# Kernel optimization log

Hardware: AMD Instinct MI355X
Metric: run time of the kernel (lower is better)

Reference implementation:

```python
import jax, jax.numpy as jnp
import numpy as np

N_WORD, N_DOC, E = 20000, 20000, 500000
H, O, D = 4, 32, 128  # heads, out per head, hidden*heads
NEG_SLOPE = 0.2


def setup_inputs() -> dict:
    key = jax.random.key(0)
    ks = jax.random.split(key, 24)
    rn = lambda k, s, sc=0.1: jax.random.normal(k, s, dtype=jnp.float32) * sc
    ri = lambda k, s, hi: jax.random.randint(k, s, 0, hi, dtype=jnp.int32)
    return {
        'x_word': rn(ks[0], (N_WORD, 300), 1.0),
        'x_doc': rn(ks[1], (N_DOC, D), 1.0),
        'Wp_word': rn(ks[2], (300, D)), 'bp_word': jnp.zeros((D,), jnp.float32),
        'Wp_doc': rn(ks[3], (D, D)), 'bp_doc': jnp.zeros((D,), jnp.float32),
        'Wsrc': rn(ks[4], (2, 3, D, D)), 'bsrc': jnp.zeros((2, 3, D), jnp.float32),
        'Wdst': rn(ks[5], (2, 3, D, D)), 'bdst': jnp.zeros((2, 3, D), jnp.float32),
        'attn': rn(ks[6], (2, 3, H, O)), 'bconv': jnp.zeros((2, 3, D), jnp.float32),
        'Wc1': rn(ks[7], (D, 64)), 'bc1': jnp.zeros((64,), jnp.float32),
        'Wc2': rn(ks[8], (64, 64)), 'bc2': jnp.zeros((64,), jnp.float32),
        'src_wd': ri(ks[9], (E,), N_WORD), 'dst_wd': ri(ks[10], (E,), N_DOC),
        'src_dw': ri(ks[11], (E,), N_DOC), 'dst_dw': ri(ks[12], (E,), N_WORD),
        'src_dd': ri(ks[13], (E,), N_DOC), 'dst_dd': ri(ks[14], (E,), N_DOC),
    }


def _gatv2(h_src, h_dst, src, dst, Ws, bs, Wd, bd, a, bias, n_dst):
    # GATv2Conv (DGL): e = a . leaky_relu(Ws h_u + Wd h_v); edge softmax per dst; sum alpha*Ws h_u
    fs = (h_src @ Ws + bs).reshape(-1, H, O)           # [N_src,H,O]
    fd = (h_dst @ Wd + bd).reshape(-1, H, O)           # [N_dst,H,O]
    e = jax.nn.leaky_relu(fs[src] + fd[dst], NEG_SLOPE)  # [E,H,O]
    score = jnp.einsum('eho,ho->eh', e, a)             # [E,H]
    m = jax.lax.stop_gradient(jax.ops.segment_max(score, dst, num_segments=n_dst))
    ex = jnp.exp(score - m[dst])
    s = jax.ops.segment_sum(ex, dst, num_segments=n_dst)
    alpha = ex / s[dst]                                 # per-dst softmax
    rst = jax.ops.segment_sum(alpha[:, :, None] * fs[src], dst, num_segments=n_dst)
    return rst + bias.reshape(1, H, O)


def reference(x_word, x_doc, Wp_word, bp_word, Wp_doc, bp_doc, Wsrc, bsrc, Wdst, bdst,
              attn, bconv, Wc1, bc1, Wc2, bc2, src_wd, dst_wd, src_dw, dst_dw, src_dd, dst_dd):
    h_w = x_word @ Wp_word + bp_word
    h_d = x_doc @ Wp_doc + bp_doc
    for l in range(2):
        o_wd = _gatv2(h_w, h_d, src_wd, dst_wd, Wsrc[l, 0], bsrc[l, 0], Wdst[l, 0], bdst[l, 0], attn[l, 0], bconv[l, 0], N_DOC)
        o_dw = _gatv2(h_d, h_w, src_dw, dst_dw, Wsrc[l, 1], bsrc[l, 1], Wdst[l, 1], bdst[l, 1], attn[l, 1], bconv[l, 1], N_WORD)
        o_dd = _gatv2(h_d, h_d, src_dd, dst_dd, Wsrc[l, 2], bsrc[l, 2], Wdst[l, 2], bdst[l, 2], attn[l, 2], bconv[l, 2], N_DOC)
        h_d = ((o_wd + o_dd) * 0.5).reshape(N_DOC, D)   # mean over 2 relations into 'document'
        h_w = o_dw.reshape(N_WORD, D)                    # mean over 1 relation into 'word'
    z = jax.nn.relu(h_d @ Wc1 + bc1)
    return z @ Wc2 + bc2  # [N_DOC, len_label]
```

## Files before the change

kernel.cpp:

```cpp
#include <hip/hip_runtime.h>

#define NNODE 20000
#define NEDGE 500000
#define CAP 64

typedef __attribute__((ext_vector_type(8))) short bf16x8;
typedef __attribute__((ext_vector_type(8))) unsigned short u16x8;
typedef __attribute__((ext_vector_type(4))) float f32x4;
typedef __attribute__((ext_vector_type(4))) int i32x4;

__device__ __forceinline__ unsigned short f2bf(float f) {
    unsigned u = __float_as_uint(f);
    return (unsigned short)((u + 0x7FFFu + ((u >> 16) & 1u)) >> 16);
}
__device__ __forceinline__ float bf2f(unsigned short h) {
    return __uint_as_float((unsigned)h << 16);
}

__device__ __forceinline__ void split_row4(
    const float* __restrict__ X, unsigned short* __restrict__ A2,
    int K, int Kp, int r, int c)
{
    float v[4];
#pragma unroll
    for (int j = 0; j < 4; ++j) v[j] = (c + j < K) ? X[(size_t)r * K + c + j] : 0.f;
    ushort4 hi, lo;
    unsigned short h;
    h = f2bf(v[0]); hi.x = h; lo.x = f2bf(v[0] - bf2f(h));
    h = f2bf(v[1]); hi.y = h; lo.y = f2bf(v[1] - bf2f(h));
    h = f2bf(v[2]); hi.z = h; lo.z = f2bf(v[2] - bf2f(h));
    h = f2bf(v[3]); hi.w = h; lo.w = f2bf(v[3] - bf2f(h));
    *reinterpret_cast<ushort4*>(A2 + (size_t)r * 2 * Kp + c) = hi;
    *reinterpret_cast<ushort4*>(A2 + (size_t)r * 2 * Kp + Kp + c) = lo;
}

__global__ __launch_bounds__(256) void split_x_kernel(
    const float* __restrict__ xw, const float* __restrict__ xd,
    unsigned short* __restrict__ Ax, unsigned short* __restrict__ Axd)
{
    int i = blockIdx.x * 256 + threadIdx.x;
    const int T1 = NNODE * 80;
    const int T2 = NNODE * 32;
    if (i < T1) {
        int r = i / 80, c = (i % 80) * 4;
        split_row4(xw, Ax, 300, 320, r, c);
    } else if (i < T1 + T2) {
        i -= T1;
        int r = i / 32, c = (i % 32) * 4;
        split_row4(xd, Axd, 128, 128, r, c);
    }
}

__device__ __forceinline__ void split_one(
    const float* __restrict__ B, unsigned short* __restrict__ Bt,
    int K, int N, int Kp, int i)
{
    int n = i / Kp, k = i % Kp;
    float v = (k < K) ? B[(size_t)k * N + n] : 0.f;
    unsigned short h = f2bf(v);
    Bt[i] = h;
    Bt[(size_t)N * Kp + i] = f2bf(v - bf2f(h));
}

__global__ __launch_bounds__(256) void prep_weights_kernel(
    const float* __restrict__ Wp_word, const float* __restrict__ Wp_doc,
    const float* __restrict__ Wsrc, const float* __restrict__ Wdst,
    const float* __restrict__ Wc1, const float* __restrict__ Wc2,
    unsigned short* __restrict__ WtPw, unsigned short* __restrict__ WtPd,
    unsigned short* __restrict__ WtCat,
    unsigned short* __restrict__ WtC1, unsigned short* __restrict__ WtC2)
{
    int i = blockIdx.x * 256 + threadIdx.x;
    const int S0 = 128 * 320, S1 = 128 * 128, S2 = 6 * 256 * 128;
    const int S3 = 64 * 128, S4 = 64 * 64;
    if (i < S0) { split_one(Wp_word, WtPw, 300, 128, 320, i); return; }
    i -= S0;
    if (i < S1) { split_one(Wp_doc, WtPd, 128, 128, 128, i); return; }
    i -= S1;
    if (i < S2) {
        int lc = i / (256 * 128), rem = i % (256 * 128);
        int n = rem / 128, k = rem % 128;
        int l = lc / 3, c = lc % 3;
        int half = n >> 7, nn = n & 127;
        const float* M;
        if (c == 0)      M = half ? (Wdst + (size_t)(l * 3 + 1) * 16384) : (Wsrc + (size_t)(l * 3 + 0) * 16384);
        else if (c == 1) M = half ? (Wsrc + (size_t)(l * 3 + 1) * 16384) : (Wdst + (size_t)(l * 3 + 0) * 16384);
        else             M = half ? (Wdst + (size_t)(l * 3 + 2) * 16384) : (Wsrc + (size_t)(l * 3 + 2) * 16384);
        float v = M[(size_t)k * 128 + nn];
        unsigned short h = f2bf(v);
        unsigned short* Bt = WtCat + (size_t)lc * 65536;
        Bt[(size_t)n * 128 + k] = h;
        Bt[32768 + (size_t)n * 128 + k] = f2bf(v - bf2f(h));
        return;
    }
    i -= S2;
    if (i < S3) { split_one(Wc1, WtC1, 128, 64, 128, i); return; }
    i -= S3;
    if (i < S4) { split_one(Wc2, WtC2, 64, 64, 64, i); }
}

template<int BM, int BN, int MODE>
__global__ __launch_bounds__(512) void gemm_mfma_kernel(
    const unsigned short* __restrict__ A2,
    const unsigned short* __restrict__ Bt,
    const float* __restrict__ b0,
    float* __restrict__ C0, unsigned short* __restrict__ S0,
    int M, int Kp, int do_relu)
{
    constexpr int FM = BM / 32;
    constexpr int FN = BN / 64;
    __shared__ unsigned short As[2][BM][40];
    __shared__ unsigned short Bs[2][BN][40];
    const int tid = threadIdx.x;
    const int m0 = blockIdx.x * BM;
    const int wid = tid >> 6, lane = tid & 63;
    const int wm = wid >> 2, wn = wid & 3;
    const int lr = lane & 15, kg = lane >> 4;

    f32x4 acc[FM][FN] = {};
    const size_t KA = 2 * (size_t)Kp;
    const size_t PB = (size_t)BN * Kp;

    for (int k0 = 0; k0 < Kp; k0 += 32) {
#pragma unroll
        for (int idx = tid; idx < BM * 4; idx += 512) {
            int row = idx >> 2, ck = idx & 3;
            u16x8 hi = {0,0,0,0,0,0,0,0}, lo = {0,0,0,0,0,0,0,0};
            if (m0 + row < M) {
                const unsigned short* ap = A2 + (size_t)(m0 + row) * KA + k0 + ck * 8;
                hi = *reinterpret_cast<const u16x8*>(ap);
                lo = *reinterpret_cast<const u16x8*>(ap + Kp);
            }
            *reinterpret_cast<u16x8*>(&As[0][row][ck * 8]) = hi;
            *reinterpret_cast<u16x8*>(&As[1][row][ck * 8]) = lo;
        }
#pragma unroll
        for (int idx = tid; idx < BN * 4; idx += 512) {
            int nr = idx >> 2, ck = idx & 3;
            const unsigned short* bp = Bt + (size_t)nr * Kp + k0 + ck * 8;
            *reinterpret_cast<u16x8*>(&Bs[0][nr][ck * 8]) = *reinterpret_cast<const u16x8*>(bp);
            *reinterpret_cast<u16x8*>(&Bs[1][nr][ck * 8]) = *reinterpret_cast<const u16x8*>(bp + PB);
        }
        __syncthreads();
        bf16x8 ah[FM], al[FM], bh[FN], bl[FN];
#pragma unroll
        for (int fm = 0; fm < FM; ++fm) {
            ah[fm] = *reinterpret_cast<const bf16x8*>(&As[0][wm * (BM / 2) + fm * 16 + lr][kg * 8]);
            al[fm] = *reinterpret_cast<const bf16x8*>(&As[1][wm * (BM / 2) + fm * 16 + lr][kg * 8]);
        }
#pragma unroll
        for (int fn = 0; fn < FN; ++fn) {
            bh[fn] = *reinterpret_cast<const bf16x8*>(&Bs[0][wn * (BN / 4) + fn * 16 + lr][kg * 8]);
            bl[fn] = *reinterpret_cast<const bf16x8*>(&Bs[1][wn * (BN / 4) + fn * 16 + lr][kg * 8]);
        }
#pragma unroll
        for (int fm = 0; fm < FM; ++fm)
#pragma unroll
            for (int fn = 0; fn < FN; ++fn) {
                acc[fm][fn] = __builtin_amdgcn_mfma_f32_16x16x32_bf16(ah[fm], bh[fn], acc[fm][fn], 0, 0, 0);
                acc[fm][fn] = __builtin_amdgcn_mfma_f32_16x16x32_bf16(al[fm], bh[fn], acc[fm][fn], 0, 0, 0);
                acc[fm][fn] = __builtin_amdgcn_mfma_f32_16x16x32_bf16(ah[fm], bl[fn], acc[fm][fn], 0, 0, 0);
            }
        __syncthreads();
    }
#pragma unroll
    for (int fm = 0; fm < FM; ++fm)
#pragma unroll
        for (int fn = 0; fn < FN; ++fn) {
            int gc = wn * (BN / 4) + fn * 16 + lr;
            float bv = b0[gc];
#pragma unroll
            for (int j = 0; j < 4; ++j) {
                int gr = m0 + wm * (BM / 2) + fm * 16 + kg * 4 + j;
                if (gr < M) {
                    float v = acc[fm][fn][j] + bv;
                    if (do_relu) v = fmaxf(v, 0.f);
                    if (MODE == 0) {
                        C0[(size_t)gr * BN + gc] = v;
                    } else {
                        unsigned short h = f2bf(v);
                        S0[(size_t)gr * 2 * BN + gc] = h;
                        S0[(size_t)gr * 2 * BN + BN + gc] = f2bf(v - bf2f(h));
                    }
                }
            }
        }
}

struct Cat3Args {
    const unsigned short* A[3];
    const unsigned short* Bt[3];
    const float* bs0[3];
    const float* bs1[3];
    unsigned short* P0[3];
    unsigned short* P1[3];
};

__global__ __launch_bounds__(512) void gemm_cat3_kernel(Cat3Args args, int M)
{
    constexpr int BM = 128, BN = 256, FM = 4, FN = 4, Kp = 128;
    const int y = blockIdx.y;
    const unsigned short* __restrict__ A2 = args.A[y];
    const unsigned short* __restrict__ Bt = args.Bt[y];
    __shared__ unsigned short As[2][BM][40];
    __shared__ unsigned short Bs[2][BN][40];
    const int tid = threadIdx.x;
    const int m0 = blockIdx.x * BM;
    const int wid = tid >> 6, lane = tid & 63;
    const int wm = wid >> 2, wn = wid & 3;
    const int lr = lane & 15, kg = lane >> 4;

    f32x4 acc[FM][FN] = {};
    const size_t KA = 2 * (size_t)Kp;
    const size_t PB = (size_t)BN * Kp;

    for (int k0 = 0; k0 < Kp; k0 += 32) {
#pragma unroll
        for (int idx = tid; idx < BM * 4; idx += 512) {
            int row = idx >> 2, ck = idx & 3;
            u16x8 hi = {0,0,0,0,0,0,0,0}, lo = {0,0,0,0,0,0,0,0};
            if (m0 + row < M) {
                const unsigned short* ap = A2 + (size_t)(m0 + row) * KA + k0 + ck * 8;
                hi = *reinterpret_cast<const u16x8*>(ap);
                lo = *reinterpret_cast<const u16x8*>(ap + Kp);
            }
            *reinterpret_cast<u16x8*>(&As[0][row][ck * 8]) = hi;
            *reinterpret_cast<u16x8*>(&As[1][row][ck * 8]) = lo;
        }
#pragma unroll
        for (int idx = tid; idx < BN * 4; idx += 512) {
            int nr = idx >> 2, ck = idx & 3;
            const unsigned short* bp = Bt + (size_t)nr * Kp + k0 + ck * 8;
            *reinterpret_cast<u16x8*>(&Bs[0][nr][ck * 8]) = *reinterpret_cast<const u16x8*>(bp);
            *reinterpret_cast<u16x8*>(&Bs[1][nr][ck * 8]) = *reinterpret_cast<const u16x8*>(bp + PB);
        }
        __syncthreads();
        bf16x8 ah[FM], al[FM], bh[FN], bl[FN];
#pragma unroll
        for (int fm = 0; fm < FM; ++fm) {
            ah[fm] = *reinterpret_cast<const bf16x8*>(&As[0][wm * 64 + fm * 16 + lr][kg * 8]);
            al[fm] = *reinterpret_cast<const bf16x8*>(&As[1][wm * 64 + fm * 16 + lr][kg * 8]);
        }
#pragma unroll
        for (int fn = 0; fn < FN; ++fn) {
            bh[fn] = *reinterpret_cast<const bf16x8*>(&Bs[0][wn * 64 + fn * 16 + lr][kg * 8]);
            bl[fn] = *reinterpret_cast<const bf16x8*>(&Bs[1][wn * 64 + fn * 16 + lr][kg * 8]);
        }
#pragma unroll
        for (int fm = 0; fm < FM; ++fm)
#pragma unroll
            for (int fn = 0; fn < FN; ++fn) {
                acc[fm][fn] = __builtin_amdgcn_mfma_f32_16x16x32_bf16(ah[fm], bh[fn], acc[fm][fn], 0, 0, 0);
                acc[fm][fn] = __builtin_amdgcn_mfma_f32_16x16x32_bf16(al[fm], bh[fn], acc[fm][fn], 0, 0, 0);
                acc[fm][fn] = __builtin_amdgcn_mfma_f32_16x16x32_bf16(ah[fm], bl[fn], acc[fm][fn], 0, 0, 0);
            }
        __syncthreads();
    }
    const float* __restrict__ bs0 = args.bs0[y];
    const float* __restrict__ bs1 = args.bs1[y];
    unsigned short* __restrict__ P0 = args.P0[y];
    unsigned short* __restrict__ P1 = args.P1[y];
#pragma unroll
    for (int fm = 0; fm < FM; ++fm)
#pragma unroll
        for (int fn = 0; fn < FN; ++fn) {
            int gc = wn * 64 + fn * 16 + lr;
            float bv = (gc < 128) ? bs0[gc] : bs1[gc - 128];
#pragma unroll
            for (int j = 0; j < 4; ++j) {
                int gr = m0 + wm * 64 + fm * 16 + kg * 4 + j;
                if (gr < M) {
                    float v = acc[fm][fn][j] + bv;
                    unsigned short h = f2bf(v);
                    if (gc < 128) P0[(size_t)gr * 128 + gc] = h;
                    else          P1[(size_t)gr * 128 + gc - 128] = h;
                }
            }
        }
}

__global__ __launch_bounds__(256) void fill_pad_kernel(
    const int* __restrict__ s0, const int* __restrict__ d0,
    const int* __restrict__ s1, const int* __restrict__ d1,
    const int* __restrict__ s2, const int* __restrict__ d2,
    int* __restrict__ deg, int* __restrict__ csr)
{
    const int QP = NEDGE / 4;
    int q = blockIdx.x * 256 + threadIdx.x;
    if (q >= 3 * QP) return;
    int rel = q / QP;
    int qi = q - rel * QP;
    const i32x4* sp = reinterpret_cast<const i32x4*>(rel == 0 ? s0 : rel == 1 ? s1 : s2);
    const i32x4* dp = reinterpret_cast<const i32x4*>(rel == 0 ? d0 : rel == 1 ? d1 : d2);
    int* dg = deg + rel * NNODE;
    int* cb = csr + (size_t)rel * NNODE * CAP;
    i32x4 d = __builtin_nontemporal_load(&dp[qi]);
    i32x4 s = __builtin_nontemporal_load(&sp[qi]);
    int c0 = atomicAdd(&dg[d.x], 1);
    int c1 = atomicAdd(&dg[d.y], 1);
    int c2 = atomicAdd(&dg[d.z], 1);
    int c3 = atomicAdd(&dg[d.w], 1);
    if (c0 < CAP) __builtin_nontemporal_store(s.x, &cb[d.x * CAP + c0]);
    if (c1 < CAP) __builtin_nontemporal_store(s.y, &cb[d.y * CAP + c1]);
    if (c2 < CAP) __builtin_nontemporal_store(s.z, &cb[d.z * CAP + c2]);
    if (c3 < CAP) __builtin_nontemporal_store(s.w, &cb[d.w * CAP + c3]);
}

__device__ __forceinline__ void rel_accum(
    const unsigned short* __restrict__ fsP,
    const unsigned short* __restrict__ fdP,
    const int* __restrict__ dg, const int* __restrict__ csrc,
    const float* __restrict__ attnRow,
    int d, int lane, float wscale, float* __restrict__ out)
{
    const int e0 = d * CAP;
    int degv = dg[d];
    if (degv > CAP) degv = CAP;
    const int e1 = e0 + degv;
    float fdv[8], av[8];
    {
        u16x8 t = *reinterpret_cast<const u16x8*>(fdP + (size_t)d * 128 + lane * 8);
#pragma unroll
        for (int j = 0; j < 8; ++j) fdv[j] = bf2f(t[j]);
    }
#pragma unroll
    for (int j = 0; j < 8; ++j) av[j] = attnRow[lane * 8 + j];

    float mx = -3.0e38f, ssum = 0.f;
    float acc[8];
#pragma unroll
    for (int j = 0; j < 8; ++j) acc[j] = 0.f;

    int i = e0;
    for (; i + 4 <= e1; i += 4) {
        int s0 = csrc[i], s1 = csrc[i + 1], s2 = csrc[i + 2], s3 = csrc[i + 3];
        u16x8 q0 = *reinterpret_cast<const u16x8*>(fsP + (size_t)s0 * 128 + lane * 8);
        u16x8 q1 = *reinterpret_cast<const u16x8*>(fsP + (size_t)s1 * 128 + lane * 8);
        u16x8 q2 = *reinterpret_cast<const u16x8*>(fsP + (size_t)s2 * 128 + lane * 8);
        u16x8 q3 = *reinterpret_cast<const u16x8*>(fsP + (size_t)s3 * 128 + lane * 8);
        float u0[8], u1[8], u2[8], u3[8];
        float p0 = 0.f, p1 = 0.f, p2 = 0.f, p3 = 0.f;
#pragma unroll
        for (int j = 0; j < 8; ++j) {
            u0[j] = bf2f(q0[j]); float v = u0[j] + fdv[j]; v = v > 0.f ? v : 0.2f * v; p0 += v * av[j];
        }
#pragma unroll
        for (int j = 0; j < 8; ++j) {
            u1[j] = bf2f(q1[j]); float v = u1[j] + fdv[j]; v = v > 0.f ? v : 0.2f * v; p1 += v * av[j];
        }
#pragma unroll
        for (int j = 0; j < 8; ++j) {
            u2[j] = bf2f(q2[j]); float v = u2[j] + fdv[j]; v = v > 0.f ? v : 0.2f * v; p2 += v * av[j];
        }
#pragma unroll
        for (int j = 0; j < 8; ++j) {
            u3[j] = bf2f(q3[j]); float v = u3[j] + fdv[j]; v = v > 0.f ? v : 0.2f * v; p3 += v * av[j];
        }
        p0 += __shfl_xor(p0, 1); p0 += __shfl_xor(p0, 2);
        p1 += __shfl_xor(p1, 1); p1 += __shfl_xor(p1, 2);
        p2 += __shfl_xor(p2, 1); p2 += __shfl_xor(p2, 2);
        p3 += __shfl_xor(p3, 1); p3 += __shfl_xor(p3, 2);
        float mnew = fmaxf(fmaxf(fmaxf(p0, p1), fmaxf(p2, p3)), mx);
        float f  = __expf(mx - mnew);
        float w0 = __expf(p0 - mnew), w1 = __expf(p1 - mnew);
        float w2 = __expf(p2 - mnew), w3 = __expf(p3 - mnew);
        ssum = ssum * f + ((w0 + w1) + (w2 + w3));
#pragma unroll
        for (int j = 0; j < 8; ++j)
            acc[j] = acc[j] * f + w0 * u0[j] + w1 * u1[j] + w2 * u2[j] + w3 * u3[j];
        mx = mnew;
    }
    for (; i < e1; ++i) {
        int s0 = csrc[i];
        u16x8 q0 = *reinterpret_cast<const u16x8*>(fsP + (size_t)s0 * 128 + lane * 8);
        float u0[8];
        float p0 = 0.f;
#pragma unroll
        for (int j = 0; j < 8; ++j) {
            u0[j] = bf2f(q0[j]); float v = u0[j] + fdv[j]; v = v > 0.f ? v : 0.2f * v; p0 += v * av[j];
        }
        p0 += __shfl_xor(p0, 1); p0 += __shfl_xor(p0, 2);
        float mnew = fmaxf(mx, p0);
        float f = __expf(mx - mnew);
        float w = __expf(p0 - mnew);
        ssum = ssum * f + w;
#pragma unroll
        for (int j = 0; j < 8; ++j) acc[j] = acc[j] * f + w * u0[j];
        mx = mnew;
    }
    float inv = (ssum > 0.f) ? wscale / ssum : 0.f;
#pragma unroll
    for (int j = 0; j < 8; ++j) out[j] += inv * acc[j];
}

__global__ __launch_bounds__(256) void gat_conv_fused_kernel(
    const unsigned short* __restrict__ fsA, const unsigned short* __restrict__ fdA,
    const int* __restrict__ degA, const int* __restrict__ csrA,
    const float* __restrict__ attnA, const float* __restrict__ biasA,
    const unsigned short* __restrict__ fsB, const unsigned short* __restrict__ fdB,
    const int* __restrict__ degB, const int* __restrict__ csrB,
    const float* __restrict__ attnB, const float* __restrict__ biasB,
    float wscale, unsigned short* __restrict__ sp, int n_dst)
{
    int gid = blockIdx.x * 256 + threadIdx.x;
    int d = gid >> 4, lane = gid & 15;
    if (d >= n_dst) return;
    float out[8];
#pragma unroll
    for (int j = 0; j < 8; ++j) {
        float b = biasA[lane * 8 + j];
        if (biasB) b += biasB[lane * 8 + j];
        out[j] = wscale * b;
    }
    rel_accum(fsA, fdA, degA, csrA, attnA, d, lane, wscale, out);
    if (fsB) rel_accum(fsB, fdB, degB, csrB, attnB, d, lane, wscale, out);
    u16x8 hv, lv;
#pragma unroll
    for (int j = 0; j < 8; ++j) {
        unsigned short h = f2bf(out[j]);
        hv[j] = h;
        lv[j] = f2bf(out[j] - bf2f(h));
    }
    *reinterpret_cast<u16x8*>(sp + (size_t)d * 256 + lane * 8) = hv;
    *reinterpret_cast<u16x8*>(sp + (size_t)d * 256 + 128 + lane * 8) = lv;
}

extern "C" void kernel_launch(void* const* d_in, const int* in_sizes, int n_in,
                              void* d_out, int out_size, void* d_ws, size_t ws_size,
                              hipStream_t stream)
{
    const float* x_word  = (const float*)d_in[0];
    const float* x_doc   = (const float*)d_in[1];
    const float* Wp_word = (const float*)d_in[2];
    const float* bp_word = (const float*)d_in[3];
    const float* Wp_doc  = (const float*)d_in[4];
    const float* bp_doc  = (const float*)d_in[5];
    const float* Wsrc    = (const float*)d_in[6];
    const float* bsrc    = (const float*)d_in[7];
    const float* Wdst    = (const float*)d_in[8];
    const float* bdst    = (const float*)d_in[9];
    const float* attn    = (const float*)d_in[10];
    const float* bconv   = (const float*)d_in[11];
    const float* Wc1     = (const float*)d_in[12];
    const float* bc1     = (const float*)d_in[13];
    const float* Wc2     = (const float*)d_in[14];
    const float* bc2     = (const float*)d_in[15];
    const int* src_wd = (const int*)d_in[16];
    const int* dst_wd = (const int*)d_in[17];
    const int* src_dw = (const int*)d_in[18];
    const int* dst_dw = (const int*)d_in[19];
    const int* src_dd = (const int*)d_in[20];
    const int* dst_dd = (const int*)d_in[21];

    const size_t NP = (size_t)NNODE * 128;
    unsigned short* U = (unsigned short*)d_ws;
    unsigned short* Pfs_wd = U;
    unsigned short* Pfd_dw = U + 1 * NP;
    unsigned short* Pfd_wd = U + 2 * NP;
    unsigned short* Pfs_dw = U + 3 * NP;
    unsigned short* Pfs_dd = U + 4 * NP;
    unsigned short* Pfd_dd = U + 5 * NP;
    unsigned short* AswA = U + 6 * NP;
    unsigned short* AsdA = AswA + 2 * NP;
    unsigned short* AswB = AsdA + 2 * NP;
    unsigned short* AsdB = AswB + 2 * NP;
    unsigned short* WtPw  = AsdB + 2 * NP;
    unsigned short* WtPd  = WtPw + 81920;
    unsigned short* WtCat = WtPd + 32768;
    unsigned short* WtC1  = WtCat + 393216;
    unsigned short* WtC2  = WtC1 + 16384;
    unsigned short* Ax  = Pfs_wd;
    unsigned short* Axd = AswB;
    unsigned short* Az  = AswB;
    int* I   = (int*)(WtC2 + 8192);
    int* deg = I;
    int* csr = I + 3 * NNODE;

    const int GB128 = (NNODE + 127) / 128;
    const int CB = (NNODE * 16 + 255) / 256;
    const int FB = (3 * (NEDGE / 4) + 255) / 256;

    (void)hipMemsetAsync(deg, 0, 3 * NNODE * sizeof(int), stream);
    fill_pad_kernel<<<FB, 256, 0, stream>>>(src_wd, dst_wd, src_dw, dst_dw,
                                            src_dd, dst_dd, deg, csr);

    prep_weights_kernel<<<(266240 + 255) / 256, 256, 0, stream>>>(
        Wp_word, Wp_doc, Wsrc, Wdst, Wc1, Wc2, WtPw, WtPd, WtCat, WtC1, WtC2);
    split_x_kernel<<<(NNODE * 112 + 255) / 256, 256, 0, stream>>>(
        x_word, x_doc, Ax, Axd);

    gemm_mfma_kernel<128, 128, 2><<<GB128, 512, 0, stream>>>(
        Ax, WtPw, bp_word, nullptr, AswA, NNODE, 320, 0);
    gemm_mfma_kernel<128, 128, 2><<<GB128, 512, 0, stream>>>(
        Axd, WtPd, bp_doc, nullptr, AsdA, NNODE, 128, 0);

    const unsigned short* Asw_in = AswA;
    const unsigned short* Asd_in = AsdA;
    for (int l = 0; l < 2; ++l) {
        const int l3 = l * 3;
        Cat3Args ca;
        ca.A[0] = Asw_in; ca.A[1] = Asd_in; ca.A[2] = Asd_in;
        ca.Bt[0] = WtCat + (size_t)(l3 + 0) * 65536;
        ca.Bt[1] = WtCat + (size_t)(l3 + 1) * 65536;
        ca.Bt[2] = WtCat + (size_t)(l3 + 2) * 65536;
        ca.bs0[0] = bsrc + (l3 + 0) * 128; ca.bs1[0] = bdst + (l3 + 1) * 128;
        ca.bs0[1] = bdst + (l3 + 0) * 128; ca.bs1[1] = bsrc + (l3 + 1) * 128;
        ca.bs0[2] = bsrc + (l3 + 2) * 128; ca.bs1[2] = bdst + (l3 + 2) * 128;
        ca.P0[0] = Pfs_wd; ca.P1[0] = Pfd_dw;
        ca.P0[1] = Pfd_wd; ca.P1[1] = Pfs_dw;
        ca.P0[2] = Pfs_dd; ca.P1[2] = Pfd_dd;
        gemm_cat3_kernel<<<dim3(GB128, 3), 512, 0, stream>>>(ca, NNODE);

        gat_conv_fused_kernel<<<CB, 256, 0, stream>>>(
            Pfs_wd, Pfd_wd, deg,             csr,                   attn + (l3 + 0) * 128, bconv + (l3 + 0) * 128,
            Pfs_dd, Pfd_dd, deg + 2 * NNODE, csr + 2 * NNODE * CAP, attn + (l3 + 2) * 128, bconv + (l3 + 2) * 128,
            0.5f, (l == 0 ? AsdB : AsdA), NNODE);
        if (l == 0) {
            gat_conv_fused_kernel<<<CB, 256, 0, stream>>>(
                Pfs_dw, Pfd_dw, deg + NNODE, csr + NNODE * CAP, attn + (l3 + 1) * 128, bconv + (l3 + 1) * 128,
                nullptr, nullptr, nullptr, nullptr, nullptr, nullptr,
                1.0f, AswB, NNODE);
        }
        Asw_in = AswB;
        Asd_in = AsdB;
    }

    gemm_mfma_kernel<128, 64, 2><<<GB128, 512, 0, stream>>>(
        AsdA, WtC1, bc1, nullptr, Az, NNODE, 128, 1);
    gemm_mfma_kernel<128, 64, 0><<<GB128, 512, 0, stream>>>(
        Az, WtC2, bc2, (float*)d_out, nullptr, NNODE, 64, 0);
}
```

Baseline: 434.8 us.

## Bucket edges by destination range before padded-CSR fill, use 16-bit CSR

Measured after the change: 428.2 us. No clear change (-1.5%).

```diff
diff --git a/kernel.cpp b/kernel.cpp
--- a/kernel.cpp
+++ b/kernel.cpp
@@ -3,11 +3,15 @@
 #define NNODE 20000
 #define NEDGE 500000
 #define CAP 64
+#define RCHUNK 2048
+#define NRANGE 8
+#define RSZ 2500
+#define SCAP 70000
+#define XW 64
 
 typedef __attribute__((ext_vector_type(8))) short bf16x8;
 typedef __attribute__((ext_vector_type(8))) unsigned short u16x8;
 typedef __attribute__((ext_vector_type(4))) float f32x4;
-typedef __attribute__((ext_vector_type(4))) int i32x4;
 
 __device__ __forceinline__ unsigned short f2bf(float f) {
     unsigned u = __float_as_uint(f);
@@ -279,37 +283,75 @@
         }
 }
 
-__global__ __launch_bounds__(256) void fill_pad_kernel(
+__global__ __launch_bounds__(256) void route_kernel(
     const int* __restrict__ s0, const int* __restrict__ d0,
     const int* __restrict__ s1, const int* __restrict__ d1,
     const int* __restrict__ s2, const int* __restrict__ d2,
-    int* __restrict__ deg, int* __restrict__ csr)
-{
-    const int QP = NEDGE / 4;
-    int q = blockIdx.x * 256 + threadIdx.x;
-    if (q >= 3 * QP) return;
-    int rel = q / QP;
-    int qi = q - rel * QP;
-    const i32x4* sp = reinterpret_cast<const i32x4*>(rel == 0 ? s0 : rel == 1 ? s1 : s2);
-    const i32x4* dp = reinterpret_cast<const i32x4*>(rel == 0 ? d0 : rel == 1 ? d1 : d2);
-    int* dg = deg + rel * NNODE;
-    int* cb = csr + (size_t)rel * NNODE * CAP;
-    i32x4 d = __builtin_nontemporal_load(&dp[qi]);
-    i32x4 s = __builtin_nontemporal_load(&sp[qi]);
-    int c0 = atomicAdd(&dg[d.x], 1);
-    int c1 = atomicAdd(&dg[d.y], 1);
-    int c2 = atomicAdd(&dg[d.z], 1);
-    int c3 = atomicAdd(&dg[d.w], 1);
-    if (c0 < CAP) __builtin_nontemporal_store(s.x, &cb[d.x * CAP + c0]);
-    if (c1 < CAP) __builtin_nontemporal_store(s.y, &cb[d.y * CAP + c1]);
-    if (c2 < CAP) __builtin_nontemporal_store(s.z, &cb[d.z * CAP + c2]);
-    if (c3 < CAP) __builtin_nontemporal_store(s.w, &cb[d.w * CAP + c3]);
+    unsigned* __restrict__ stage, int* __restrict__ scur)
+{
+    __shared__ unsigned sbuf[RCHUNK];
+    __shared__ int hcnt[NRANGE], hoff[NRANGE], gbase[NRANGE], hcur[NRANGE];
+    const int rel = blockIdx.y;
+    const int c0 = blockIdx.x * RCHUNK;
+    const int n = (c0 + RCHUNK <= NEDGE) ? RCHUNK : (NEDGE - c0);
+    const int tid = threadIdx.x;
+    const int* sp = rel == 0 ? s0 : rel == 1 ? s1 : s2;
+    const int* dp = rel == 0 ? d0 : rel == 1 ? d1 : d2;
+
+    if (tid < NRANGE) hcnt[tid] = 0;
+    __syncthreads();
+    for (int i = tid; i < n; i += 256) atomicAdd(&hcnt[dp[c0 + i] / RSZ], 1);
+    __syncthreads();
+    if (tid == 0) {
+        int o = 0;
+        for (int r = 0; r < NRANGE; ++r) {
+            hoff[r] = o; hcur[r] = o; o += hcnt[r];
+            gbase[r] = atomicAdd(&scur[rel * NRANGE + r], hcnt[r]);
+        }
+    }
+    __syncthreads();
+    for (int i = tid; i < n; i += 256) {
+        int d = dp[c0 + i], s = sp[c0 + i];
+        int k = atomicAdd(&hcur[d / RSZ], 1);
+        sbuf[k] = ((unsigned)d << 16) | (unsigned)s;
+    }
+    __syncthreads();
+    for (int r = 0; r < NRANGE; ++r) {
+        int cnt = hcnt[r];
+        int lim = SCAP - gbase[r];
+        if (cnt > lim) cnt = lim;
+        unsigned* dst = stage + (size_t)(rel * NRANGE + r) * SCAP + gbase[r];
+        for (int i = tid; i < cnt; i += 256) dst[i] = sbuf[hoff[r] + i];
+    }
+}
+
+__global__ __launch_bounds__(256) void xfill_kernel(
+    const unsigned* __restrict__ stage, const int* __restrict__ scur,
+    int* __restrict__ deg, unsigned short* __restrict__ csr)
+{
+    const int r = blockIdx.x & 7;
+    const int w = blockIdx.x >> 3;
+    const int tid = threadIdx.x;
+#pragma unroll
+    for (int rel = 0; rel < 3; ++rel) {
+        int total = scur[rel * NRANGE + r];
+        if (total > SCAP) total = SCAP;
+        const unsigned* st = stage + (size_t)(rel * NRANGE + r) * SCAP;
+        int* dg = deg + rel * NNODE;
+        unsigned short* cb = csr + (size_t)rel * NNODE * CAP;
+        for (int i = w * 256 + tid; i < total; i += XW * 256) {
+            unsigned p = st[i];
+            int d = (int)(p >> 16), s = (int)(p & 0xFFFFu);
+            int k = atomicAdd(&dg[d], 1);
+            if (k < CAP) cb[(size_t)d * CAP + k] = (unsigned short)s;
+        }
+    }
 }
 
 __device__ __forceinline__ void rel_accum(
     const unsigned short* __restrict__ fsP,
     const unsigned short* __restrict__ fdP,
-    const int* __restrict__ dg, const int* __restrict__ csrc,
+    const int* __restrict__ dg, const unsigned short* __restrict__ csrc,
     const float* __restrict__ attnRow,
     int d, int lane, float wscale, float* __restrict__ out)
 {
@@ -395,10 +437,10 @@
 
 __global__ __launch_bounds__(256) void gat_conv_fused_kernel(
     const unsigned short* __restrict__ fsA, const unsigned short* __restrict__ fdA,
-    const int* __restrict__ degA, const int* __restrict__ csrA,
+    const int* __restrict__ degA, const unsigned short* __restrict__ csrA,
     const float* __restrict__ attnA, const float* __restrict__ biasA,
     const unsigned short* __restrict__ fsB, const unsigned short* __restrict__ fdB,
-    const int* __restrict__ degB, const int* __restrict__ csrB,
+    const int* __restrict__ degB, const unsigned short* __restrict__ csrB,
     const float* __restrict__ attnB, const float* __restrict__ biasB,
     float wscale, unsigned short* __restrict__ sp, int n_dst)
 {
@@ -472,17 +514,20 @@
     unsigned short* Ax  = Pfs_wd;
     unsigned short* Axd = AswB;
     unsigned short* Az  = AswB;
-    int* I   = (int*)(WtC2 + 8192);
-    int* deg = I;
-    int* csr = I + 3 * NNODE;
+    int* I    = (int*)(WtC2 + 8192);
+    int* deg  = I;
+    int* scur = I + 3 * NNODE;
+    unsigned* stage = (unsigned*)(scur + 32);
+    unsigned short* csrp = (unsigned short*)(stage + 3 * NRANGE * SCAP);
 
     const int GB128 = (NNODE + 127) / 128;
     const int CB = (NNODE * 16 + 255) / 256;
-    const int FB = (3 * (NEDGE / 4) + 255) / 256;
-
-    (void)hipMemsetAsync(deg, 0, 3 * NNODE * sizeof(int), stream);
-    fill_pad_kernel<<<FB, 256, 0, stream>>>(src_wd, dst_wd, src_dw, dst_dw,
-                                            src_dd, dst_dd, deg, csr);
+    const int RB = (NEDGE + RCHUNK - 1) / RCHUNK;
+
+    (void)hipMemsetAsync(deg, 0, (3 * NNODE + 32) * sizeof(int), stream);
+    route_kernel<<<dim3(RB, 3), 256, 0, stream>>>(
+        src_wd, dst_wd, src_dw, dst_dw, src_dd, dst_dd, stage, scur);
+    xfill_kernel<<<NRANGE * XW, 256, 0, stream>>>(stage, scur, deg, csrp);
 
     prep_weights_kernel<<<(266240 + 255) / 256, 256, 0, stream>>>(
         Wp_word, Wp_doc, Wsrc, Wdst, Wc1, Wc2, WtPw, WtPd, WtCat, WtC1, WtC2);
@@ -512,12 +557,12 @@
         gemm_cat3_kernel<<<dim3(GB128, 3), 512, 0, stream>>>(ca, NNODE);
 
         gat_conv_fused_kernel<<<CB, 256, 0, stream>>>(
-            Pfs_wd, Pfd_wd, deg,             csr,                   attn + (l3 + 0) * 128, bconv + (l3 + 0) * 128,
-            Pfs_dd, Pfd_dd, deg + 2 * NNODE, csr + 2 * NNODE * CAP, attn + (l3 + 2) * 128, bconv + (l3 + 2) * 128,
+            Pfs_wd, Pfd_wd, deg,             csrp,                   attn + (l3 + 0) * 128, bconv + (l3 + 0) * 128,
+            Pfs_dd, Pfd_dd, deg + 2 * NNODE, csrp + (size_t)2 * NNODE * CAP, attn + (l3 + 2) * 128, bconv + (l3 + 2) * 128,
             0.5f, (l == 0 ? AsdB : AsdA), NNODE);
         if (l == 0) {
             gat_conv_fused_kernel<<<CB, 256, 0, stream>>>(
-                Pfs_dw, Pfd_dw, deg + NNODE, csr + NNODE * CAP, attn + (l3 + 1) * 128, bconv + (l3 + 1) * 128,
+                Pfs_dw, Pfd_dw, deg + NNODE, csrp + (size_t)NNODE * CAP, attn + (l3 + 1) * 128, bconv + (l3 + 1) * 128,
                 nullptr, nullptr, nullptr, nullptr, nullptr, nullptr,
                 1.0f, AswB, NNODE);
         }
```
